# Optimization experiments

Measured on AMD Instinct MI355X. Metric: run time of the kernel, lower is better.

## Reference

```python
import jax, jax.numpy as jnp
import numpy as np

B, S, H, DFF, HOP = 64, 512, 512, 2048, 6
THRESHOLD = 1.0 - 0.1  # self.threshold in the torch module


def setup_inputs() -> dict:
    key = jax.random.key(0)
    k = jax.random.split(key, 8)
    sc = 0.02
    return {
        "state": jax.random.normal(k[0], (B, S, H), jnp.float32),
        "inputs": jax.random.normal(k[1], (B, S, H), jnp.float32),
        "time_enc": jax.random.normal(k[2], (1, S, H), jnp.float32) * sc,
        "pos_enc": jax.random.normal(k[3], (1, HOP, H), jnp.float32) * sc,
        "w_p": jax.random.normal(k[4], (H,), jnp.float32) * sc,
        "b_p": jnp.ones((1,), jnp.float32),  # p.bias.data.fill_(1)
        "w1": jax.random.normal(k[5], (H, DFF), jnp.float32) * sc,
        "b1": jnp.zeros((DFF,), jnp.float32),
        "w2": jax.random.normal(k[6], (DFF, H), jnp.float32) * sc,
        "b2": jnp.zeros((H,), jnp.float32),
        "max_hop": HOP,
    }


def reference(state, inputs, time_enc, pos_enc, w_p, b_p, w1, b1, w2, b2, max_hop):
    Bv, Sv, Hv = inputs.shape
    dt = state.dtype
    zeros_bs = jnp.zeros((Bv, Sv), dt)

    def step(carry, pos_t):
        st, halting, remainders, n_updates, prev = carry
        # time + per-step positional signal
        st = st + time_enc[:, :Sv, :] + pos_t[None, None, :]
        # halting probability p = sigmoid(Linear(state)) -> [B,S]
        p = jax.nn.sigmoid(jnp.einsum('bsh,h->bs', st, w_p) + b_p[0])
        still = (halting < 1.0).astype(dt)
        cand = halting + p * still
        new_halted = (cand > THRESHOLD).astype(dt) * still
        still = (cand <= THRESHOLD).astype(dt) * still
        halting = halting + p * still
        remainders = remainders + new_halted * (1.0 - halting)
        halting = halting + new_halted * remainders
        n_updates = n_updates + still + new_halted
        uw = (p * still + new_halted * remainders)[..., None]  # update weights
        # fn(state): wrapped transformer sublayer, here a dense FFN
        st = jnp.maximum(st @ w1 + b1, 0.0) @ w2 + b2
        prev = st * uw + prev * (1.0 - uw)
        return (st, halting, remainders, n_updates, prev), None

    init = (state, zeros_bs, zeros_bs, zeros_bs, jnp.zeros_like(inputs))
    # Fixed max_hop iterations: once a position halts, still/new_halted are 0
    # and all its bookkeeping + blended state are exact no-ops, so this matches
    # the data-dependent torch while-loop exactly.
    (st, halting, remainders, n_updates, prev), _ = jax.lax.scan(
        step, init, pos_enc[0, :max_hop])
    return prev, remainders, n_updates
```

## Files before the change

kernel.cpp:

```cpp
#include <hip/hip_runtime.h>
#include <math.h>

typedef short short8 __attribute__((ext_vector_type(8)));
typedef _Float16 half8 __attribute__((ext_vector_type(8)));
typedef float floatx4 __attribute__((ext_vector_type(4)));

#define Bb 64
#define Ss 512
#define Hh 512
#define DFF 2048
#define HOPS 6
#define BS (Bb*Ss)
#define PS 1048576
#define BUFA 8192

__device__ inline unsigned short f16u(float v) {
  _Float16 h = (_Float16)v;
  union { _Float16 h; unsigned short u; } c; c.h = h; return c.u;
}
__device__ inline void split8_store1(const float* xs, unsigned short* dst) {
  unsigned q[4];
#pragma unroll
  for (int j = 0; j < 4; ++j)
    q[j] = (unsigned)f16u(xs[2*j]) | ((unsigned)f16u(xs[2*j+1]) << 16);
  *(int4*)dst = make_int4(q[0], q[1], q[2], q[3]);
}

__device__ __forceinline__ void gload16(const void* g, void* l) {
  __builtin_amdgcn_global_load_lds(
      (const __attribute__((address_space(1))) void*)g,
      (__attribute__((address_space(3))) void*)l, 16, 0, 0);
}

__global__ __launch_bounds__(256) void prep_kernel(
    const float* __restrict__ w, unsigned short* __restrict__ wf,
    int K32, int NTOT, int N)
{
  int id = blockIdx.x * 256 + threadIdx.x;
  if (id >= K32 * NTOT * 64) return;
  int l  = id & 63;
  int NT = (id >> 6) % NTOT;
  int k0 = id / (64 * NTOT);
  int n  = NT * 16 + (l & 15);
  int kb = k0 * 32 + 8 * (l >> 4);
  float xs[8];
#pragma unroll
  for (int j = 0; j < 8; ++j) xs[j] = w[(size_t)(kb + j) * N + n];
  split8_store1(xs, wf + (size_t)id * 8);
}

__global__ __launch_bounds__(1024) void compact_kernel(
    const float* __restrict__ halting, int* __restrict__ idx,
    int* __restrict__ cnt, int tzero)
{
  __shared__ int wsum[16];
  __shared__ int wbase[16];
  __shared__ int s_base;
  int tid = threadIdx.x;
  int lane = tid & 63, wid = tid >> 6;
  int pos = blockIdx.x * 1024 + tid;
  int flag = tzero ? 1 : ((halting[pos] < 1.0f) ? 1 : 0);
  unsigned long long m = __ballot(flag);
  int pre = __popcll(m & ((1ull << lane) - 1ull));
  if (lane == 0) wsum[wid] = __popcll(m);
  __syncthreads();
  if (tid == 0) {
    int a = 0;
#pragma unroll
    for (int i = 0; i < 16; ++i) { wbase[i] = a; a += wsum[i]; }
    s_base = (a > 0) ? atomicAdd(cnt, a) : 0;
  }
  __syncthreads();
  if (flag) idx[s_base + wbase[wid] + pre] = pos;
}

__global__ __launch_bounds__(256) void halt_kernel(
    const float* __restrict__ st, const float* __restrict__ te,
    const float* __restrict__ pe_t, const float* __restrict__ wp,
    const float* __restrict__ bp, float* __restrict__ halting,
    float* __restrict__ remainders, float* __restrict__ n_updates,
    float* __restrict__ uw_c, const int* __restrict__ idxbuf,
    const int* __restrict__ cntp, int tzero)
{
  int cnt = *cntp;
  int i = blockIdx.x * 4 + (threadIdx.x >> 6);
  if (i >= cnt) return;
  int lane = threadIdx.x & 63;
  int pos = idxbuf[i];
  int s = pos & (Ss - 1);
  const float4* stv = (const float4*)(st + (size_t)pos * Hh);
  const float4* tev = (const float4*)(te + (size_t)s * Hh);
  const float4* pev = (const float4*)pe_t;
  const float4* wpv = (const float4*)wp;
  float sum = 0.f;
#pragma unroll
  for (int j = 0; j < 2; ++j) {
    int idx = lane + j * 64;
    float4 a = stv[idx], b = tev[idx], c = pev[idx], w = wpv[idx];
    sum += (a.x + b.x + c.x) * w.x + (a.y + b.y + c.y) * w.y +
           (a.z + b.z + c.z) * w.z + (a.w + b.w + c.w) * w.w;
  }
#pragma unroll
  for (int off = 32; off > 0; off >>= 1) sum += __shfl_xor(sum, off, 64);
  if (lane == 0) {
    float y = sum + bp[0];
    float p = 1.0f / (1.0f + expf(-y));
    const float THRESH = 1.0f - 0.1f;
    float h0  = tzero ? 0.f : halting[pos];
    float rem = tzero ? 0.f : remainders[pos];
    float nup = tzero ? 0.f : n_updates[pos];
    float still = (h0 < 1.0f) ? 1.f : 0.f;
    float cand  = h0 + p * still;
    float nh  = ((cand >  THRESH) ? 1.f : 0.f) * still;
    float st2 = ((cand <= THRESH) ? 1.f : 0.f) * still;
    h0  += p * st2;
    rem += nh * (1.0f - h0);
    h0  += nh * rem;
    nup += st2 + nh;
    float uwv = p * st2 + nh * rem;
    halting[pos]    = h0;
    remainders[pos] = rem;
    n_updates[pos]  = nup;
    uw_c[i]         = uwv;
  }
}

__global__ __launch_bounds__(256) void stagex_kernel(
    const float* __restrict__ st, const float* __restrict__ te,
    const float* __restrict__ pe_t, unsigned short* __restrict__ xf,
    const int* __restrict__ idxbuf, const int* __restrict__ cntp,
    int m_base, int mrows)
{
  const int K32 = Hh / 32;
  int cnt = *cntp;
  int rel = cnt - m_base;
  if (rel <= 0) return;
  if (rel > mrows) rel = mrows;
  int rows_pad = (rel + 127) & ~127;
  if (rows_pad > mrows) rows_pad = mrows;
  int id = blockIdx.x * 256 + threadIdx.x;
  int l = id & 63;
  int f = id >> 6;
  int mtile = f / K32, k0 = f - mtile * K32;
  if (mtile * 16 >= rows_pad) return;
  int m = m_base + mtile * 16 + (l & 15);
  int mc = (m < cnt) ? m : cnt - 1;
  int pos = idxbuf[mc];
  int kb = k0 * 32 + (l >> 4) * 8;
  const float* ap = st + (size_t)pos * Hh + kb;
  const float* tp = te + (size_t)(pos & (Ss - 1)) * Hh + kb;
  const float* pp = pe_t + kb;
  float4 xa = *(const float4*)ap, xb = *(const float4*)(ap + 4);
  float4 ta = *(const float4*)tp, tb = *(const float4*)(tp + 4);
  float4 pa = *(const float4*)pp, pb = *(const float4*)(pp + 4);
  float xs[8];
  xs[0] = xa.x + ta.x + pa.x; xs[1] = xa.y + ta.y + pa.y;
  xs[2] = xa.z + ta.z + pa.z; xs[3] = xa.w + ta.w + pa.w;
  xs[4] = xb.x + tb.x + pb.x; xs[5] = xb.y + tb.y + pb.y;
  xs[6] = xb.z + tb.z + pb.z; xs[7] = xb.w + tb.w + pb.w;
  split8_store1(xs, xf + ((size_t)f * 64 + l) * 8);
}


#define LSTR 66
__global__ __launch_bounds__(256, 3) void gemm1_kernel(
    const unsigned short* __restrict__ xf, const unsigned short* __restrict__ w1f,
    const float* __restrict__ b1, unsigned short* __restrict__ hf,
    const int* __restrict__ cntp, int m_base)
{
  __shared__ __align__(1024) char stage[3 * BUFA];
  const int K32 = Hh / 32, NTOT = DFF / 16;
  int lin = blockIdx.x;
  int gsz = gridDim.x;
  int q = gsz >> 3, r = gsz & 7;
  int xcd = lin & 7, idx0 = lin >> 3;
  int swz = (xcd < r) ? (xcd * (q + 1) + idx0)
                      : (r * (q + 1) + (xcd - r) * q + idx0);
  int strip = swz >> 4;
  int nb    = swz & 15;
  int cnt = *cntp;
  int m0 = strip * 128;
  if (m_base + m0 >= cnt) return;
  int tid = threadIdx.x, lane = tid & 63, w = tid >> 6;
  int wm = w >> 1, wn = w & 1;
  int n0 = nb * 128;
  int mtb0 = m0 >> 4, ntb0 = n0 >> 4;
  char* sptr = stage;

  auto stageA = [&](int bsel, int kk) {
    unsigned so = (unsigned)bsel * (unsigned)BUFA;
#pragma unroll
    for (int j = 0; j < 2; ++j) {
      int u = w * 2 + j;
      const unsigned short* g =
          xf + ((size_t)(mtb0 + u) * K32 + kk) * 512 + (size_t)lane * 8;
      gload16(g, sptr + so + (unsigned)u * 1024u);
    }
  };
  auto loadB = [&](half8 (&b)[4], int kk) {
#pragma unroll
    for (int nt = 0; nt < 4; ++nt)
      b[nt] = *(const half8*)(w1f +
          ((size_t)kk * NTOT + (ntb0 + wn * 4 + nt)) * 512 + (size_t)lane * 8);
  };

  floatx4 am[4][4];
#pragma unroll
  for (int i = 0; i < 4; ++i)
#pragma unroll
    for (int j = 0; j < 4; ++j) am[i][j] = (floatx4){0.f, 0.f, 0.f, 0.f};

  half8 bfA[4], bfB[4];
  stageA(0, 0);
  loadB(bfA, 0);

  auto iter = [&](int k, int cur, half8 (&bu)[4], half8 (&bl)[4]) -> int {
    int nxt = (cur == 2) ? 0 : cur + 1;
    if (k + 1 < K32) {
      stageA(nxt, k + 1);
      loadB(bl, k + 1);
      asm volatile("s_waitcnt vmcnt(6)" ::: "memory");
    } else {
      asm volatile("s_waitcnt vmcnt(0)" ::: "memory");
    }
    __builtin_amdgcn_s_barrier();
    asm volatile("" ::: "memory");
    const char* sb = sptr + cur * BUFA + (size_t)lane * 16;
    half8 af[4];
#pragma unroll
    for (int mt = 0; mt < 4; ++mt)
      af[mt] = *(const half8*)(sb + (wm * 4 + mt) * 1024);
    __builtin_amdgcn_s_setprio(1);
#pragma unroll
    for (int mt = 0; mt < 4; ++mt)
#pragma unroll
      for (int nt = 0; nt < 4; ++nt)
        am[mt][nt] = __builtin_amdgcn_mfma_f32_16x16x32_f16(af[mt], bu[nt],
                                                            am[mt][nt], 0, 0, 0);
    __builtin_amdgcn_s_setprio(0);
    asm volatile("" ::: "memory");
    return nxt;
  };

  int cur = 0;
  for (int k0 = 0; k0 < K32; k0 += 2) {
    cur = iter(k0,     cur, bfA, bfB);
    cur = iter(k0 + 1, cur, bfB, bfA);
  }
  __syncthreads();
  {
    int r0 = (lane >> 4) * 4;
    int c0l = lane & 15;
    int mtb = mtb0 + wm * 4;
    int k2b = (n0 >> 5) + wn * 2;
    float* L = (float*)(void*)sptr + (size_t)w * (16 * LSTR);
    float bias[4];
#pragma unroll
    for (int nt = 0; nt < 4; ++nt) bias[nt] = b1[n0 + wn * 64 + nt * 16 + c0l];
#pragma unroll
    for (int mt = 0; mt < 4; ++mt) {
#pragma unroll
      for (int nt = 0; nt < 4; ++nt)
#pragma unroll
        for (int reg = 0; reg < 4; ++reg)
          L[(r0 + reg) * LSTR + nt * 16 + c0l] =
              fmaxf(am[mt][nt][reg] + bias[nt], 0.f);
#pragma unroll
      for (int k2 = 0; k2 < 2; ++k2) {
        const float* rp = L + (lane & 15) * LSTR + k2 * 32 + (lane >> 4) * 8;
        float xs[8];
        float4 xa = *(const float4*)rp, xb = *(const float4*)(rp + 4);
        xs[0]=xa.x; xs[1]=xa.y; xs[2]=xa.z; xs[3]=xa.w;
        xs[4]=xb.x; xs[5]=xb.y; xs[6]=xb.z; xs[7]=xb.w;
        size_t f2 = (size_t)(mtb + mt) * 64 + (k2b + k2);
        split8_store1(xs, hf + (f2 * 64 + lane) * 8);
      }
    }
  }
}

__global__ __launch_bounds__(256, 3) void gemm2f_kernel(
    const unsigned short* __restrict__ hf, const unsigned short* __restrict__ w2f,
    const float* __restrict__ b2, const float* __restrict__ uw_c,
    float* __restrict__ st_out, float* __restrict__ prev,
    const int* __restrict__ idxbuf, const int* __restrict__ cntp,
    int m_base, int tzero)
{
  __shared__ __align__(1024) char stage[3 * BUFA];
  const int K32 = DFF / 32, NTOT = Hh / 16;
  int lin = blockIdx.x;
  int gsz = gridDim.x;
  int q = gsz >> 3, r = gsz & 7;
  int xcd = lin & 7, idx0 = lin >> 3;
  int swz = (xcd < r) ? (xcd * (q + 1) + idx0)
                      : (r * (q + 1) + (xcd - r) * q + idx0);
  int strip = swz >> 2, nb = swz & 3;
  int cnt = *cntp;
  int m0 = strip * 128;
  if (m_base + m0 >= cnt) return;
  int n0 = nb * 128;
  int tid = threadIdx.x, lane = tid & 63, w = tid >> 6;
  int wm = w >> 1, wn = w & 1;
  int mtb0 = m0 >> 4, ntb0 = n0 >> 4;
  char* sptr = stage;

  auto stageA = [&](int bsel, int kk) {
    unsigned so = (unsigned)bsel * (unsigned)BUFA;
#pragma unroll
    for (int j = 0; j < 2; ++j) {
      int u = w * 2 + j;
      const unsigned short* g =
          hf + ((size_t)(mtb0 + u) * K32 + kk) * 512 + (size_t)lane * 8;
      gload16(g, sptr + so + (unsigned)u * 1024u);
    }
  };
  auto loadB = [&](half8 (&b)[4], int kk) {
#pragma unroll
    for (int nt = 0; nt < 4; ++nt)
      b[nt] = *(const half8*)(w2f +
          ((size_t)kk * NTOT + (ntb0 + wn * 4 + nt)) * 512 + (size_t)lane * 8);
  };

  floatx4 am[4][4];
#pragma unroll
  for (int i = 0; i < 4; ++i)
#pragma unroll
    for (int j = 0; j < 4; ++j) am[i][j] = (floatx4){0.f, 0.f, 0.f, 0.f};

  half8 bfA[4], bfB[4];
  stageA(0, 0);
  loadB(bfA, 0);

  auto iter = [&](int k, int cur, half8 (&bu)[4], half8 (&bl)[4]) -> int {
    int nxt = (cur == 2) ? 0 : cur + 1;
    if (k + 1 < K32) {
      stageA(nxt, k + 1);
      loadB(bl, k + 1);
      asm volatile("s_waitcnt vmcnt(6)" ::: "memory");
    } else {
      asm volatile("s_waitcnt vmcnt(0)" ::: "memory");
    }
    __builtin_amdgcn_s_barrier();
    asm volatile("" ::: "memory");
    const char* sb = sptr + cur * BUFA + (size_t)lane * 16;
    half8 af[4];
#pragma unroll
    for (int mt = 0; mt < 4; ++mt)
      af[mt] = *(const half8*)(sb + (wm * 4 + mt) * 1024);
#pragma unroll
    for (int mt = 0; mt < 4; ++mt)
#pragma unroll
      for (int nt = 0; nt < 4; ++nt)
        am[mt][nt] = __builtin_amdgcn_mfma_f32_16x16x32_f16(af[mt], bu[nt],
                                                            am[mt][nt], 0, 0, 0);
    asm volatile("" ::: "memory");
    return nxt;
  };

  int cur = 0;
  for (int k0 = 0; k0 < K32; k0 += 2) {
    cur = iter(k0,     cur, bfA, bfB);
    cur = iter(k0 + 1, cur, bfB, bfA);
  }
  {
    int r0 = (lane >> 4) * 4;
    int c0l = lane & 15;
    int mtb = mtb0 + wm * 4;
    int njb = ntb0 + wn * 4;
    float bias[4];
#pragma unroll
    for (int nt = 0; nt < 4; ++nt) bias[nt] = b2[(njb + nt) * 16 + c0l];
#pragma unroll
    for (int mt = 0; mt < 4; ++mt) {
      int pos4[4]; float uw4[4]; bool ok4[4];
#pragma unroll
      for (int reg = 0; reg < 4; ++reg) {
        int m = m_base + (mtb + mt) * 16 + r0 + reg;
        ok4[reg] = (m < cnt);
        int mc = ok4[reg] ? m : 0;
        pos4[reg] = idxbuf[mc];
        uw4[reg]  = uw_c[mc];
      }
#pragma unroll
      for (int nt = 0; nt < 4; ++nt) {
        int col = (njb + nt) * 16 + c0l;
#pragma unroll
        for (int reg = 0; reg < 4; ++reg) {
          if (ok4[reg]) {
            float sv = am[mt][nt][reg] + bias[nt];
            size_t off = (size_t)pos4[reg] * Hh + col;
            float pv = tzero ? 0.f : prev[off];
            st_out[off] = sv;
            prev[off] = sv * uw4[reg] + pv * (1.f - uw4[reg]);
          }
        }
      }
    }
  }
}

extern "C" void kernel_launch(void* const* d_in, const int* in_sizes, int n_in,
                              void* d_out, int out_size, void* d_ws, size_t ws_size,
                              hipStream_t stream) {
  const float* state  = (const float*)d_in[0];
  const float* te     = (const float*)d_in[2];
  const float* pe     = (const float*)d_in[3];
  const float* wp     = (const float*)d_in[4];
  const float* bp     = (const float*)d_in[5];
  const float* w1     = (const float*)d_in[6];
  const float* b1     = (const float*)d_in[7];
  const float* w2     = (const float*)d_in[8];
  const float* b2     = (const float*)d_in[9];

  float* out        = (float*)d_out;
  float* prev       = out;
  float* remainders = out + (size_t)BS * Hh;
  float* n_updates  = remainders + BS;

  float*          st      = (float*)d_ws;
  float*          halting = st + (size_t)BS * Hh;
  float*          uw_c    = halting + BS;
  int*            idxbuf  = (int*)(uw_c + BS);
  int*            cntp    = idxbuf + BS;
  unsigned short* w1f     = (unsigned short*)(cntp + 64);
  unsigned short* w2f     = w1f + (size_t)PS;
  unsigned short* hf      = w2f + (size_t)PS;

  size_t fixed = (size_t)((char*)hf - (char*)d_ws);
  size_t avail = (ws_size > fixed) ? (ws_size - fixed) : 0;
  int hrows = (int)((avail / 5120) & ~(size_t)127);
  if (hrows > BS) hrows = BS;
  if (hrows < 128) hrows = 128;
  unsigned short* xf = hf + (size_t)hrows * DFF;
  int nst = hrows / 128;

  hipMemsetAsync(cntp, 0, 64 * sizeof(int), stream);

  prep_kernel<<<512, 256, 0, stream>>>(w1, w1f, Hh / 32, DFF / 16, DFF);
  prep_kernel<<<512, 256, 0, stream>>>(w2, w2f, DFF / 32, Hh / 16, Hh);

  for (int t = 0; t < HOPS; ++t) {
    const float* pe_t = pe + (size_t)t * Hh;
    int* cnt_t = cntp + t;
    int tz = (t == 0) ? 1 : 0;
    const float* st_src = tz ? state : st;
    compact_kernel<<<BS / 1024, 1024, 0, stream>>>(halting, idxbuf, cnt_t, tz);
    halt_kernel<<<BS / 4, 256, 0, stream>>>(st_src, te, pe_t, wp, bp, halting,
                                            remainders, n_updates, uw_c,
                                            idxbuf, cnt_t, tz);
    for (int mb = 0; mb < BS; mb += hrows) {
      stagex_kernel<<<hrows / 4, 256, 0, stream>>>(st_src, te, pe_t, xf, idxbuf,
                                                   cnt_t, mb, hrows);
      gemm1_kernel<<<nst * 16, 256, 0, stream>>>(xf, w1f, b1, hf, cnt_t, mb);
      gemm2f_kernel<<<nst * 4, 256, 0, stream>>>(hf, w2f, b2, uw_c, st, prev,
                                                 idxbuf, cnt_t, mb, tz);
    }
  }
}
```

Before: 566.7 us.

## Load GEMM A fragments directly from global memory into registers, dropping LDS staging

Both FFN GEMM kernels stop staging A tiles through a triple-buffered LDS ring via global_load_lds and barriers. Each wave now loads its A fragments straight from global memory into registers, double-buffered alongside B. This removes per-k-step barriers and LDS traffic and frees shared memory. In exchange, A tiles that were shared across the two N-waves are now fetched twice from global/L2, register pressure rises, and the setprio hints are gone.

```diff
diff --git a/kernel.cpp b/kernel.cpp
--- a/kernel.cpp
+++ b/kernel.cpp
@@ -12,7 +12,6 @@
 #define HOPS 6
 #define BS (Bb*Ss)
 #define PS 1048576
-#define BUFA 8192
 
 __device__ inline unsigned short f16u(float v) {
   _Float16 h = (_Float16)v;
@@ -24,12 +23,6 @@
   for (int j = 0; j < 4; ++j)
     q[j] = (unsigned)f16u(xs[2*j]) | ((unsigned)f16u(xs[2*j+1]) << 16);
   *(int4*)dst = make_int4(q[0], q[1], q[2], q[3]);
-}
-
-__device__ __forceinline__ void gload16(const void* g, void* l) {
-  __builtin_amdgcn_global_load_lds(
-      (const __attribute__((address_space(1))) void*)g,
-      (__attribute__((address_space(3))) void*)l, 16, 0, 0);
 }
 
 __global__ __launch_bounds__(256) void prep_kernel(
@@ -168,7 +161,7 @@
     const float* __restrict__ b1, unsigned short* __restrict__ hf,
     const int* __restrict__ cntp, int m_base)
 {
-  __shared__ __align__(1024) char stage[3 * BUFA];
+  __shared__ __align__(16) float L4[4][16 * LSTR];
   const int K32 = Hh / 32, NTOT = DFF / 16;
   int lin = blockIdx.x;
   int gsz = gridDim.x;
@@ -185,17 +178,12 @@
   int wm = w >> 1, wn = w & 1;
   int n0 = nb * 128;
   int mtb0 = m0 >> 4, ntb0 = n0 >> 4;
-  char* sptr = stage;
-
-  auto stageA = [&](int bsel, int kk) {
-    unsigned so = (unsigned)bsel * (unsigned)BUFA;
-#pragma unroll
-    for (int j = 0; j < 2; ++j) {
-      int u = w * 2 + j;
-      const unsigned short* g =
-          xf + ((size_t)(mtb0 + u) * K32 + kk) * 512 + (size_t)lane * 8;
-      gload16(g, sptr + so + (unsigned)u * 1024u);
-    }
+
+  auto loadA = [&](half8 (&a)[4], int kk) {
+#pragma unroll
+    for (int mt = 0; mt < 4; ++mt)
+      a[mt] = *(const half8*)(xf +
+          ((size_t)(mtb0 + wm * 4 + mt) * K32 + kk) * 512 + (size_t)lane * 8);
   };
   auto loadB = [&](half8 (&b)[4], int kk) {
 #pragma unroll
@@ -210,50 +198,30 @@
 #pragma unroll
     for (int j = 0; j < 4; ++j) am[i][j] = (floatx4){0.f, 0.f, 0.f, 0.f};
 
-  half8 bfA[4], bfB[4];
-  stageA(0, 0);
-  loadB(bfA, 0);
-
-  auto iter = [&](int k, int cur, half8 (&bu)[4], half8 (&bl)[4]) -> int {
-    int nxt = (cur == 2) ? 0 : cur + 1;
-    if (k + 1 < K32) {
-      stageA(nxt, k + 1);
-      loadB(bl, k + 1);
-      asm volatile("s_waitcnt vmcnt(6)" ::: "memory");
-    } else {
-      asm volatile("s_waitcnt vmcnt(0)" ::: "memory");
-    }
-    __builtin_amdgcn_s_barrier();
-    asm volatile("" ::: "memory");
-    const char* sb = sptr + cur * BUFA + (size_t)lane * 16;
-    half8 af[4];
-#pragma unroll
-    for (int mt = 0; mt < 4; ++mt)
-      af[mt] = *(const half8*)(sb + (wm * 4 + mt) * 1024);
-    __builtin_amdgcn_s_setprio(1);
+  half8 aP[4], bP[4], aQ[4], bQ[4];
+  loadA(aP, 0); loadB(bP, 0);
+  for (int k0 = 0; k0 < K32; k0 += 2) {
+    if (k0 + 1 < K32) { loadA(aQ, k0 + 1); loadB(bQ, k0 + 1); }
 #pragma unroll
     for (int mt = 0; mt < 4; ++mt)
 #pragma unroll
       for (int nt = 0; nt < 4; ++nt)
-        am[mt][nt] = __builtin_amdgcn_mfma_f32_16x16x32_f16(af[mt], bu[nt],
+        am[mt][nt] = __builtin_amdgcn_mfma_f32_16x16x32_f16(aP[mt], bP[nt],
                                                             am[mt][nt], 0, 0, 0);
-    __builtin_amdgcn_s_setprio(0);
-    asm volatile("" ::: "memory");
-    return nxt;
-  };
-
-  int cur = 0;
-  for (int k0 = 0; k0 < K32; k0 += 2) {
-    cur = iter(k0,     cur, bfA, bfB);
-    cur = iter(k0 + 1, cur, bfB, bfA);
-  }
-  __syncthreads();
+    if (k0 + 2 < K32) { loadA(aP, k0 + 2); loadB(bP, k0 + 2); }
+#pragma unroll
+    for (int mt = 0; mt < 4; ++mt)
+#pragma unroll
+      for (int nt = 0; nt < 4; ++nt)
+        am[mt][nt] = __builtin_amdgcn_mfma_f32_16x16x32_f16(aQ[mt], bQ[nt],
+                                                            am[mt][nt], 0, 0, 0);
+  }
   {
     int r0 = (lane >> 4) * 4;
     int c0l = lane & 15;
     int mtb = mtb0 + wm * 4;
     int k2b = (n0 >> 5) + wn * 2;
-    float* L = (float*)(void*)sptr + (size_t)w * (16 * LSTR);
+    float* L = &L4[w][0];
     float bias[4];
 #pragma unroll
     for (int nt = 0; nt < 4; ++nt) bias[nt] = b1[n0 + wn * 64 + nt * 16 + c0l];
@@ -286,7 +254,6 @@
     const int* __restrict__ idxbuf, const int* __restrict__ cntp,
     int m_base, int tzero)
 {
-  __shared__ __align__(1024) char stage[3 * BUFA];
   const int K32 = DFF / 32, NTOT = Hh / 16;
   int lin = blockIdx.x;
   int gsz = gridDim.x;
@@ -302,17 +269,12 @@
   int tid = threadIdx.x, lane = tid & 63, w = tid >> 6;
   int wm = w >> 1, wn = w & 1;
   int mtb0 = m0 >> 4, ntb0 = n0 >> 4;
-  char* sptr = stage;
-
-  auto stageA = [&](int bsel, int kk) {
-    unsigned so = (unsigned)bsel * (unsigned)BUFA;
-#pragma unroll
-    for (int j = 0; j < 2; ++j) {
-      int u = w * 2 + j;
-      const unsigned short* g =
-          hf + ((size_t)(mtb0 + u) * K32 + kk) * 512 + (size_t)lane * 8;
-      gload16(g, sptr + so + (unsigned)u * 1024u);
-    }
+
+  auto loadA = [&](half8 (&a)[4], int kk) {
+#pragma unroll
+    for (int mt = 0; mt < 4; ++mt)
+      a[mt] = *(const half8*)(hf +
+          ((size_t)(mtb0 + wm * 4 + mt) * K32 + kk) * 512 + (size_t)lane * 8);
   };
   auto loadB = [&](half8 (&b)[4], int kk) {
 #pragma unroll
@@ -327,40 +289,23 @@
 #pragma unroll
     for (int j = 0; j < 4; ++j) am[i][j] = (floatx4){0.f, 0.f, 0.f, 0.f};
 
-  half8 bfA[4], bfB[4];
-  stageA(0, 0);
-  loadB(bfA, 0);
-
-  auto iter = [&](int k, int cur, half8 (&bu)[4], half8 (&bl)[4]) -> int {
-    int nxt = (cur == 2) ? 0 : cur + 1;
-    if (k + 1 < K32) {
-      stageA(nxt, k + 1);
-      loadB(bl, k + 1);
-      asm volatile("s_waitcnt vmcnt(6)" ::: "memory");
-    } else {
-      asm volatile("s_waitcnt vmcnt(0)" ::: "memory");
-    }
-    __builtin_amdgcn_s_barrier();
-    asm volatile("" ::: "memory");
-    const char* sb = sptr + cur * BUFA + (size_t)lane * 16;
-    half8 af[4];
-#pragma unroll
-    for (int mt = 0; mt < 4; ++mt)
-      af[mt] = *(const half8*)(sb + (wm * 4 + mt) * 1024);
+  half8 aP[4], bP[4], aQ[4], bQ[4];
+  loadA(aP, 0); loadB(bP, 0);
+  for (int k0 = 0; k0 < K32; k0 += 2) {
+    if (k0 + 1 < K32) { loadA(aQ, k0 + 1); loadB(bQ, k0 + 1); }
 #pragma unroll
     for (int mt = 0; mt < 4; ++mt)
 #pragma unroll
       for (int nt = 0; nt < 4; ++nt)
-        am[mt][nt] = __builtin_amdgcn_mfma_f32_16x16x32_f16(af[mt], bu[nt],
+        am[mt][nt] = __builtin_amdgcn_mfma_f32_16x16x32_f16(aP[mt], bP[nt],
                                                             am[mt][nt], 0, 0, 0);
-    asm volatile("" ::: "memory");
-    return nxt;
-  };
-
-  int cur = 0;
-  for (int k0 = 0; k0 < K32; k0 += 2) {
-    cur = iter(k0,     cur, bfA, bfB);
-    cur = iter(k0 + 1, cur, bfB, bfA);
+    if (k0 + 2 < K32) { loadA(aP, k0 + 2); loadB(bP, k0 + 2); }
+#pragma unroll
+    for (int mt = 0; mt < 4; ++mt)
+#pragma unroll
+      for (int nt = 0; nt < 4; ++nt)
+        am[mt][nt] = __builtin_amdgcn_mfma_f32_16x16x32_f16(aQ[mt], bQ[nt],
+                                                            am[mt][nt], 0, 0, 0);
   }
   {
     int r0 = (lane >> 4) * 4;
```

Measured after the change: 751.9 us. +32.7%, slower.
